# Kernel optimization log

Measured on AMD Instinct MI355X. Metric: run time of the kernel, lower is better.

The kernel has to match this reference:

```python
import jax, jax.numpy as jnp
import numpy as np

B, T, C, H = 2, 2048, 1024, 16
HD = C // H  # head_size = 64
EPS = 1e-5


def setup_inputs() -> dict:
    key = jax.random.key(0)
    ks = jax.random.split(key, 12)
    s = lambda fan_in: 1.0 / np.sqrt(fan_in)
    return {
        "x": jax.random.normal(ks[0], (B, T, C), jnp.float32),
        # attention projections, stored [in, out] so y = x @ W
        "Wq": jax.random.normal(ks[1], (C, C), jnp.float32) * s(C),
        "Wk": jax.random.normal(ks[2], (C, C), jnp.float32) * s(C),
        "Wv": jax.random.normal(ks[3], (C, C), jnp.float32) * s(C),
        "Wo": jax.random.normal(ks[4], (C, C), jnp.float32) * s(C),
        "bo": jnp.zeros((C,), jnp.float32),
        "ln1_g": jnp.ones((C,), jnp.float32),
        "ln1_b": jnp.zeros((C,), jnp.float32),
        "ln2_g": jnp.ones((C,), jnp.float32),
        "ln2_b": jnp.zeros((C,), jnp.float32),
        "W1": jax.random.normal(ks[5], (C, 4 * C), jnp.float32) * s(C),
        "b1": jnp.zeros((4 * C,), jnp.float32),
        "W2": jax.random.normal(ks[6], (4 * C, C), jnp.float32) * s(4 * C),
        "b2": jnp.zeros((C,), jnp.float32),
    }


def _layernorm(x, g, b):
    mu = jnp.mean(x, axis=-1, keepdims=True)
    var = jnp.mean(jnp.square(x - mu), axis=-1, keepdims=True)
    return (x - mu) * jax.lax.rsqrt(var + EPS) * g + b


def reference(x, Wq, Wk, Wv, Wo, bo, ln1_g, ln1_b, ln2_g, ln2_b, W1, b1, W2, b2):
    # Dropout layers are inference no-ops (eval mode).
    Bz, Tz, Cz = x.shape
    h = _layernorm(x, ln1_g, ln1_b)
    # fused multi-head projections (equivalent to per-head Linears concatenated)
    q = (h @ Wq).reshape(Bz, Tz, H, HD)
    k = (h @ Wk).reshape(Bz, Tz, H, HD)
    v = (h @ Wv).reshape(Bz, Tz, H, HD)
    scores = jnp.einsum("bqhd,bkhd->bhqk", q, k) / np.sqrt(HD).astype(np.float32)
    causal = jnp.tril(jnp.ones((Tz, Tz), bool))
    scores = jnp.where(causal, scores, -jnp.inf)
    attn = jax.nn.softmax(scores, axis=-1)
    out = jnp.einsum("bhqk,bkhd->bqhd", attn, v).reshape(Bz, Tz, Cz)
    x = x + out @ Wo + bo
    h2 = _layernorm(x, ln2_g, ln2_b)
    ff = jax.nn.relu(h2 @ W1 + b1) @ W2 + b2
    return x + ff
```

## Files before the change

kernel.cpp:

```cpp
#include <hip/hip_runtime.h>
#include <hip/hip_bf16.h>
#include <stdint.h>

#define B_  2
#define T_  2048
#define C_  1024
#define H_  16
#define HD_ 64
#define M_  4096
#define FF_ 4096

typedef unsigned short ushort_t;
typedef __bf16 bf16x8 __attribute__((ext_vector_type(8)));
typedef float  f32x4  __attribute__((ext_vector_type(4)));
typedef float  f32x16 __attribute__((ext_vector_type(16)));
typedef unsigned int u32x2 __attribute__((ext_vector_type(2)));
typedef unsigned int u32x4 __attribute__((ext_vector_type(4)));

#define C2_ 0.1803368801111204f

__device__ inline ushort_t f2bf(float f) {
  uint32_t u = __builtin_bit_cast(uint32_t, f);
  u += 0x7fffu + ((u >> 16) & 1u);
  return (ushort_t)(u >> 16);
}
__device__ inline uint32_t pk2(float lo, float hi) {
  return (uint32_t)f2bf(lo) | ((uint32_t)f2bf(hi) << 16);
}

__device__ inline void gload_lds16(const void* g, void* l) {
  __builtin_amdgcn_global_load_lds(
      (const __attribute__((address_space(1))) uint32_t*)g,
      (__attribute__((address_space(3))) uint32_t*)l, 16, 0, 0);
}

__device__ inline int qswz(int row, int byte_in_row) {
  return row * 128 + (byte_in_row ^ ((row & 7) << 4));
}

__global__ __launch_bounds__(256) void lnorm_kernel(
    const float* __restrict__ x, const float* __restrict__ g,
    const float* __restrict__ b, ushort_t* __restrict__ o) {
  int row = blockIdx.x;
  int tid = threadIdx.x;
  const float4* xr = (const float4*)(x + (size_t)row * C_);
  float4 xv = xr[tid];
  float s  = xv.x + xv.y + xv.z + xv.w;
  float s2 = xv.x*xv.x + xv.y*xv.y + xv.z*xv.z + xv.w*xv.w;
#pragma unroll
  for (int off = 32; off; off >>= 1) {
    s  += __shfl_down(s,  off);
    s2 += __shfl_down(s2, off);
  }
  __shared__ float rs[4], rq[4];
  int wid = tid >> 6;
  if ((tid & 63) == 0) { rs[wid] = s; rq[wid] = s2; }
  __syncthreads();
  float tot  = rs[0] + rs[1] + rs[2] + rs[3];
  float tot2 = rq[0] + rq[1] + rq[2] + rq[3];
  float mu   = tot * (1.0f / C_);
  float var  = tot2 * (1.0f / C_) - mu * mu;
  float rstd = rsqrtf(var + 1e-5f);
  float4 gv = ((const float4*)g)[tid];
  float4 bv = ((const float4*)b)[tid];
  float y0 = (xv.x - mu) * rstd * gv.x + bv.x;
  float y1 = (xv.y - mu) * rstd * gv.y + bv.y;
  float y2 = (xv.z - mu) * rstd * gv.z + bv.z;
  float y3 = (xv.w - mu) * rstd * gv.w + bv.w;
  uint2 pk;
  pk.x = (uint32_t)f2bf(y0) | ((uint32_t)f2bf(y1) << 16);
  pk.y = (uint32_t)f2bf(y2) | ((uint32_t)f2bf(y3) << 16);
  *(uint2*)(o + (size_t)row * C_ + tid * 4) = pk;
}

__global__ __launch_bounds__(256) void tcast_kernel(
    const float* __restrict__ W, ushort_t* __restrict__ Wt, int K, int N) {
  __shared__ float t[32][33];
  int bn = blockIdx.x, bk = blockIdx.y;
  int tx = threadIdx.x & 31, ty = threadIdx.x >> 5;
#pragma unroll
  for (int i = 0; i < 4; ++i)
    t[ty + i*8][tx] = W[(size_t)(bk*32 + ty + i*8) * N + bn*32 + tx];
  __syncthreads();
#pragma unroll
  for (int i = 0; i < 4; ++i)
    Wt[(size_t)(bn*32 + ty + i*8) * K + bk*32 + tx] = f2bf(t[tx][ty + i*8]);
}

__global__ __launch_bounds__(256) void vtrans_kernel(
    const ushort_t* __restrict__ qkv, ushort_t* __restrict__ vt) {
  __shared__ ushort_t t[32][33];
  int tt = blockIdx.x;
  int cc = blockIdx.y;
  int bb = blockIdx.z;
  int tx = threadIdx.x & 31, ty = threadIdx.x >> 5;
#pragma unroll
  for (int i = 0; i < 4; ++i)
    t[ty + i*8][tx] = qkv[(size_t)(bb*T_ + tt*32 + ty + i*8)*3072 + 2048 + cc*32 + tx];
  __syncthreads();
  int crow = threadIdx.x >> 4;
  int ucol = threadIdx.x & 15;
#pragma unroll
  for (int i = 0; i < 2; ++i) {
    int c = crow + i*16;
    uint32_t vlo = t[ucol*2][c], vhi = t[ucol*2 + 1][c];
    *(uint32_t*)&vt[(size_t)(bb*1024 + cc*32 + c)*T_ + tt*32 + ucol*2] =
        vlo | (vhi << 16);
  }
}

template<int BIAS, int RELU, int RESID, int OUTBF16>
__global__ __launch_bounds__(256) void gemm_kernel(
    const ushort_t* __restrict__ A, const ushort_t* __restrict__ Bt,
    const float* __restrict__ bias, const float* __restrict__ resid,
    void* __restrict__ outp, int M, int N, int K) {
  __shared__ __align__(16) ushort_t As[128*32];
  __shared__ __align__(16) ushort_t Bs[128*32];
  int bn = blockIdx.x, bm = blockIdx.y;
  int tid = threadIdx.x;
  int lane = tid & 63, wid = tid >> 6;
  int wr = (wid >> 1) * 64, wc = (wid & 1) * 64;
  int r = lane & 15, g = lane >> 4;
  int srow = tid >> 2, scc = (tid & 3) * 8;
  int srow2 = srow + 64;
  f32x4 acc[4][4] = {};
  int nk = K >> 5;
  for (int kt = 0; kt < nk; ++kt) {
    gload_lds16(&A[(size_t)(bm*128 + srow)  * K + kt*32 + scc], &As[tid*8]);
    gload_lds16(&A[(size_t)(bm*128 + srow2) * K + kt*32 + scc], &As[(tid+256)*8]);
    gload_lds16(&Bt[(size_t)(bn*128 + srow)  * K + kt*32 + scc], &Bs[tid*8]);
    gload_lds16(&Bt[(size_t)(bn*128 + srow2) * K + kt*32 + scc], &Bs[(tid+256)*8]);
    __syncthreads();
    bf16x8 af[4], bfv[4];
#pragma unroll
    for (int m = 0; m < 4; ++m)
      af[m] = *(const bf16x8*)&As[(wr + m*16 + r)*32 + g*8];
#pragma unroll
    for (int n = 0; n < 4; ++n)
      bfv[n] = *(const bf16x8*)&Bs[(wc + n*16 + r)*32 + g*8];
#pragma unroll
    for (int m = 0; m < 4; ++m)
#pragma unroll
      for (int n = 0; n < 4; ++n)
        acc[m][n] = __builtin_amdgcn_mfma_f32_16x16x32_bf16(
            af[m], bfv[n], acc[m][n], 0, 0, 0);
    __syncthreads();
  }
#pragma unroll
  for (int m = 0; m < 4; ++m)
#pragma unroll
    for (int n = 0; n < 4; ++n)
#pragma unroll
      for (int e = 0; e < 4; ++e) {
        int row = bm*128 + wr + m*16 + g*4 + e;
        int col = bn*128 + wc + n*16 + r;
        float v = acc[m][n][e];
        if (BIAS)  v += bias[col];
        if (RESID) v += resid[(size_t)row * N + col];
        if (RELU)  v = fmaxf(v, 0.0f);
        if (OUTBF16) ((ushort_t*)outp)[(size_t)row * N + col] = f2bf(v);
        else         ((float*)outp)[(size_t)row * N + col]    = v;
      }
}

__global__ __launch_bounds__(256) void attn_kernel(
    const ushort_t* __restrict__ q, const ushort_t* __restrict__ k,
    const ushort_t* __restrict__ vt, ushort_t* __restrict__ o, int ldq) {
  int bid = blockIdx.x;
  int qbb = 15 - (bid & 15);
  int hh = (bid >> 4) & 15;
  int bb = bid >> 8;
  __shared__ __align__(16) ushort_t Ks[64*64];
  __shared__ __align__(16) ushort_t Vts[64*64];
  int tid = threadIdx.x, lane = tid & 63, w = tid >> 6;
  int qi = lane & 31, hi = lane >> 5;
  int qrow0 = qbb*128 + w*32;
  int qg = qrow0 + qi;
  int lt = 2*qbb + (w >> 1);
  int nkv = 2*qbb + 2;

  const ushort_t* qbase = q + ((size_t)(bb*T_ + qg))*ldq + hh*64;
  bf16x8 qv[4];
#pragma unroll
  for (int c = 0; c < 4; ++c)
    qv[c] = *(const bf16x8*)(qbase + c*16 + hi*8);

  const ushort_t* kbase = k  + ((size_t)bb*T_)*ldq + hh*64;
  const ushort_t* vbase = vt + ((size_t)(bb*1024 + hh*64))*T_;

  int r0s = tid >> 3;
  int s0  = ((tid & 7) ^ (r0s & 7)) * 8;

  f32x16 O0 = {}, O1 = {};
  float mrun = -1e30f, lrun = 0.f;

  for (int kt = 0; kt < nkv; ++kt) {
    gload_lds16(kbase + ((size_t)(kt*64 + r0s))*ldq + s0,      &Ks[tid*8]);
    gload_lds16(kbase + ((size_t)(kt*64 + r0s + 32))*ldq + s0, &Ks[(tid+256)*8]);
    gload_lds16(vbase + (size_t)r0s*T_ + kt*64 + s0,           &Vts[tid*8]);
    gload_lds16(vbase + (size_t)(r0s+32)*T_ + kt*64 + s0,      &Vts[(tid+256)*8]);
    __syncthreads();
    if (kt <= lt) {
      f32x16 a0 = {}, a1 = {};
#pragma unroll
      for (int c = 0; c < 4; ++c) {
        bf16x8 k0 = *(const bf16x8*)((char*)Ks + qswz(qi,      c*32 + hi*16));
        bf16x8 k1 = *(const bf16x8*)((char*)Ks + qswz(32 + qi, c*32 + hi*16));
        a0 = __builtin_amdgcn_mfma_f32_32x32x16_bf16(k0, qv[c], a0, 0, 0, 0);
        a1 = __builtin_amdgcn_mfma_f32_32x32x16_bf16(k1, qv[c], a1, 0, 0, 0);
      }
      if (kt == lt) {
        int kof = kt*64 + 4*hi;
#pragma unroll
        for (int rg = 0; rg < 16; ++rg) {
          int kp = kof + (rg & 3) + 8*(rg >> 2);
          if (kp > qg)      a0[rg] = -1e30f;
          if (kp + 32 > qg) a1[rg] = -1e30f;
        }
      }
      float tm = -1e30f;
#pragma unroll
      for (int rg = 0; rg < 16; ++rg) tm = fmaxf(tm, fmaxf(a0[rg], a1[rg]));
      tm = fmaxf(tm, __shfl_xor(tm, 32));
      float mnew = fmaxf(mrun, tm);
      float sf = exp2f((mrun - mnew) * C2_);
      mrun = mnew;
      float mc = mnew * C2_;
#pragma unroll
      for (int rg = 0; rg < 16; ++rg) {
        a0[rg] = exp2f(a0[rg]*C2_ - mc);
        a1[rg] = exp2f(a1[rg]*C2_ - mc);
      }
      float rs = 0.f;
#pragma unroll
      for (int rg = 0; rg < 16; ++rg) rs += a0[rg] + a1[rg];
      rs += __shfl_xor(rs, 32);
      lrun = lrun*sf + rs;
#pragma unroll
      for (int rg = 0; rg < 16; ++rg) { O0[rg] *= sf; O1[rg] *= sf; }
      bf16x8 pf[4];
#pragma unroll
      for (int kb = 0; kb < 2; ++kb)
#pragma unroll
        for (int jj = 0; jj < 2; ++jj) {
          int rb = jj*8;
          float v0 = kb ? a1[rb+0] : a0[rb+0], v1 = kb ? a1[rb+1] : a0[rb+1];
          float v2 = kb ? a1[rb+2] : a0[rb+2], v3 = kb ? a1[rb+3] : a0[rb+3];
          float v4 = kb ? a1[rb+4] : a0[rb+4], v5 = kb ? a1[rb+5] : a0[rb+5];
          float v6 = kb ? a1[rb+6] : a0[rb+6], v7 = kb ? a1[rb+7] : a0[rb+7];
          uint32_t d0 = pk2(v0, v1), d1 = pk2(v2, v3);
          uint32_t e0 = pk2(v4, v5), e1 = pk2(v6, v7);
          uint32_t pd0 = __shfl_xor(d0, 32), pd1 = __shfl_xor(d1, 32);
          uint32_t pe0 = __shfl_xor(e0, 32), pe1 = __shfl_xor(e1, 32);
          u32x4 fw;
          fw[0] = hi ? pe0 : d0;
          fw[1] = hi ? pe1 : d1;
          fw[2] = hi ? e0  : pd0;
          fw[3] = hi ? e1  : pd1;
          pf[kb*2 + jj] = __builtin_bit_cast(bf16x8, fw);
        }
#pragma unroll
      for (int kk = 0; kk < 4; ++kk) {
        bf16x8 vv0 = *(const bf16x8*)((char*)Vts + qswz(qi,      kk*32 + hi*16));
        bf16x8 vv1 = *(const bf16x8*)((char*)Vts + qswz(32 + qi, kk*32 + hi*16));
        O0 = __builtin_amdgcn_mfma_f32_32x32x16_bf16(vv0, pf[kk], O0, 0, 0, 0);
        O1 = __builtin_amdgcn_mfma_f32_32x32x16_bf16(vv1, pf[kk], O1, 0, 0, 0);
      }
    }
    __syncthreads();
  }
  float inv = 1.0f / lrun;
  ushort_t* ob = o + ((size_t)(bb*T_ + qg))*C_ + hh*64;
#pragma unroll
  for (int tq = 0; tq < 4; ++tq) {
    u32x2 st0, st1;
    st0[0] = pk2(O0[4*tq+0]*inv, O0[4*tq+1]*inv);
    st0[1] = pk2(O0[4*tq+2]*inv, O0[4*tq+3]*inv);
    st1[0] = pk2(O1[4*tq+0]*inv, O1[4*tq+1]*inv);
    st1[1] = pk2(O1[4*tq+2]*inv, O1[4*tq+3]*inv);
    *(u32x2*)(ob + 8*tq + 4*hi)      = st0;
    *(u32x2*)(ob + 32 + 8*tq + 4*hi) = st1;
  }
}

extern "C" void kernel_launch(void* const* d_in, const int* in_sizes, int n_in,
                              void* d_out, int out_size, void* d_ws, size_t ws_size,
                              hipStream_t stream) {
  const float* x    = (const float*)d_in[0];
  const float* Wq   = (const float*)d_in[1];
  const float* Wk   = (const float*)d_in[2];
  const float* Wv   = (const float*)d_in[3];
  const float* Wo   = (const float*)d_in[4];
  const float* bo   = (const float*)d_in[5];
  const float* ln1g = (const float*)d_in[6];
  const float* ln1b = (const float*)d_in[7];
  const float* ln2g = (const float*)d_in[8];
  const float* ln2b = (const float*)d_in[9];
  const float* W1   = (const float*)d_in[10];
  const float* b1   = (const float*)d_in[11];
  const float* W2   = (const float*)d_in[12];
  const float* b2   = (const float*)d_in[13];

  char* ws = (char*)d_ws;
  ushort_t* h    = (ushort_t*)(ws + ((size_t)0  << 20));
  ushort_t* vt   = (ushort_t*)(ws + ((size_t)0  << 20));
  ushort_t* qkv  = (ushort_t*)(ws + ((size_t)8  << 20));
  ushort_t* ff   = (ushort_t*)(ws + ((size_t)0  << 20));
  ushort_t* attn = (ushort_t*)(ws + ((size_t)32 << 20));
  float*    x2   = (float*)   (ws + ((size_t)40 << 20));
  ushort_t* h2   = (ushort_t*)(ws + ((size_t)56 << 20));
  ushort_t* wqt  = (ushort_t*)(ws + ((size_t)64 << 20));
  ushort_t* wkt  = (ushort_t*)(ws + ((size_t)66 << 20));
  ushort_t* wvt  = (ushort_t*)(ws + ((size_t)68 << 20));
  ushort_t* wot  = (ushort_t*)(ws + ((size_t)70 << 20));
  ushort_t* w1t  = (ushort_t*)(ws + ((size_t)72 << 20));
  ushort_t* w2t  = (ushort_t*)(ws + ((size_t)80 << 20));
  float* out = (float*)d_out;

  tcast_kernel<<<dim3(32, 32),  256, 0, stream>>>(Wq, wqt, 1024, 1024);
  tcast_kernel<<<dim3(32, 32),  256, 0, stream>>>(Wk, wkt, 1024, 1024);
  tcast_kernel<<<dim3(32, 32),  256, 0, stream>>>(Wv, wvt, 1024, 1024);
  tcast_kernel<<<dim3(32, 32),  256, 0, stream>>>(Wo, wot, 1024, 1024);
  tcast_kernel<<<dim3(128, 32), 256, 0, stream>>>(W1, w1t, 1024, 4096);
  tcast_kernel<<<dim3(32, 128), 256, 0, stream>>>(W2, w2t, 4096, 1024);

  lnorm_kernel<<<M_, 256, 0, stream>>>(x, ln1g, ln1b, h);

  gemm_kernel<0,0,0,1><<<dim3(24, 32), 256, 0, stream>>>(h, wqt, nullptr, nullptr, qkv, M_, 3*C_, C_);

  vtrans_kernel<<<dim3(64, 32, 2), 256, 0, stream>>>(qkv, vt);

  attn_kernel<<<512, 256, 0, stream>>>(qkv, qkv + C_, vt, attn, 3*C_);

  gemm_kernel<1,0,1,0><<<dim3(8, 32), 256, 0, stream>>>(attn, wot, bo, x, x2, M_, C_, C_);

  lnorm_kernel<<<M_, 256, 0, stream>>>(x2, ln2g, ln2b, h2);

  gemm_kernel<1,1,0,1><<<dim3(32, 32), 256, 0, stream>>>(h2, w1t, b1, nullptr, ff, M_, FF_, C_);

  gemm_kernel<1,0,1,0><<<dim3(8, 32), 256, 0, stream>>>(ff, w2t, b2, x2, out, M_, C_, FF_);
}
```

Before: 457.0 us.

## Double-buffer GEMM LDS tiles and use narrower N tiles for C-output GEMMs

The GEMM kernel now keeps two LDS buffers and issues the global-to-LDS loads for the next K tile before computing on the current one, so load latency can overlap with MFMA work and one barrier per iteration is dropped. A BN template parameter lets the two GEMMs with 1024 output columns use 64-wide N tiles, which doubles their grid from 256 to 512 blocks to fill more CUs. The cost is double the LDS per block, which may lower occupancy, and less reuse of the A tile in the narrow-tile case.

```diff
diff --git a/kernel.cpp b/kernel.cpp
--- a/kernel.cpp
+++ b/kernel.cpp
@@ -109,51 +109,68 @@
   }
 }
 
-template<int BIAS, int RELU, int RESID, int OUTBF16>
+template<int BN, int BIAS, int RELU, int RESID, int OUTBF16>
 __global__ __launch_bounds__(256) void gemm_kernel(
     const ushort_t* __restrict__ A, const ushort_t* __restrict__ Bt,
     const float* __restrict__ bias, const float* __restrict__ resid,
     void* __restrict__ outp, int M, int N, int K) {
-  __shared__ __align__(16) ushort_t As[128*32];
-  __shared__ __align__(16) ushort_t Bs[128*32];
+  constexpr int NFR = BN / 32;
+  __shared__ __align__(16) ushort_t As[2][128*32];
+  __shared__ __align__(16) ushort_t Bs[2][BN*32];
   int bn = blockIdx.x, bm = blockIdx.y;
   int tid = threadIdx.x;
   int lane = tid & 63, wid = tid >> 6;
-  int wr = (wid >> 1) * 64, wc = (wid & 1) * 64;
+  int wr = (wid >> 1) * 64, wc = (wid & 1) * (BN / 2);
   int r = lane & 15, g = lane >> 4;
   int srow = tid >> 2, scc = (tid & 3) * 8;
-  int srow2 = srow + 64;
-  f32x4 acc[4][4] = {};
+  f32x4 acc[4][NFR] = {};
   int nk = K >> 5;
+
+  const ushort_t* Abase = A  + (size_t)(bm*128) * K;
+  const ushort_t* Bbase = Bt + (size_t)(bn*BN) * K;
+
+#define STAGE_(bi, kt_)                                                        \
+  do {                                                                         \
+    gload_lds16(Abase + (size_t)srow * K + (kt_)*32 + scc, &As[bi][tid*8]);    \
+    gload_lds16(Abase + (size_t)(srow + 64) * K + (kt_)*32 + scc,              \
+                &As[bi][(tid + 256)*8]);                                       \
+    gload_lds16(Bbase + (size_t)srow * K + (kt_)*32 + scc, &Bs[bi][tid*8]);    \
+    if (BN == 128)                                                             \
+      gload_lds16(Bbase + (size_t)(srow + 64) * K + (kt_)*32 + scc,            \
+                  &Bs[bi][(tid + 256)*8]);                                     \
+  } while (0)
+
+  STAGE_(0, 0);
+  __syncthreads();
+  int buf = 0;
   for (int kt = 0; kt < nk; ++kt) {
-    gload_lds16(&A[(size_t)(bm*128 + srow)  * K + kt*32 + scc], &As[tid*8]);
-    gload_lds16(&A[(size_t)(bm*128 + srow2) * K + kt*32 + scc], &As[(tid+256)*8]);
-    gload_lds16(&Bt[(size_t)(bn*128 + srow)  * K + kt*32 + scc], &Bs[tid*8]);
-    gload_lds16(&Bt[(size_t)(bn*128 + srow2) * K + kt*32 + scc], &Bs[(tid+256)*8]);
-    __syncthreads();
-    bf16x8 af[4], bfv[4];
+    if (kt + 1 < nk) STAGE_(buf ^ 1, kt + 1);
+    bf16x8 af[4], bfv[NFR];
 #pragma unroll
     for (int m = 0; m < 4; ++m)
-      af[m] = *(const bf16x8*)&As[(wr + m*16 + r)*32 + g*8];
-#pragma unroll
-    for (int n = 0; n < 4; ++n)
-      bfv[n] = *(const bf16x8*)&Bs[(wc + n*16 + r)*32 + g*8];
+      af[m] = *(const bf16x8*)&As[buf][(wr + m*16 + r)*32 + g*8];
+#pragma unroll
+    for (int n = 0; n < NFR; ++n)
+      bfv[n] = *(const bf16x8*)&Bs[buf][(wc + n*16 + r)*32 + g*8];
 #pragma unroll
     for (int m = 0; m < 4; ++m)
 #pragma unroll
-      for (int n = 0; n < 4; ++n)
+      for (int n = 0; n < NFR; ++n)
         acc[m][n] = __builtin_amdgcn_mfma_f32_16x16x32_bf16(
             af[m], bfv[n], acc[m][n], 0, 0, 0);
     __syncthreads();
-  }
+    buf ^= 1;
+  }
+#undef STAGE_
+
 #pragma unroll
   for (int m = 0; m < 4; ++m)
 #pragma unroll
-    for (int n = 0; n < 4; ++n)
+    for (int n = 0; n < NFR; ++n)
 #pragma unroll
       for (int e = 0; e < 4; ++e) {
         int row = bm*128 + wr + m*16 + g*4 + e;
-        int col = bn*128 + wc + n*16 + r;
+        int col = bn*BN + wc + n*16 + r;
         float v = acc[m][n][e];
         if (BIAS)  v += bias[col];
         if (RESID) v += resid[(size_t)row * N + col];
@@ -326,17 +343,17 @@
 
   lnorm_kernel<<<M_, 256, 0, stream>>>(x, ln1g, ln1b, h);
 
-  gemm_kernel<0,0,0,1><<<dim3(24, 32), 256, 0, stream>>>(h, wqt, nullptr, nullptr, qkv, M_, 3*C_, C_);
+  gemm_kernel<128,0,0,0,1><<<dim3(24, 32), 256, 0, stream>>>(h, wqt, nullptr, nullptr, qkv, M_, 3*C_, C_);
 
   vtrans_kernel<<<dim3(64, 32, 2), 256, 0, stream>>>(qkv, vt);
 
   attn_kernel<<<512, 256, 0, stream>>>(qkv, qkv + C_, vt, attn, 3*C_);
 
-  gemm_kernel<1,0,1,0><<<dim3(8, 32), 256, 0, stream>>>(attn, wot, bo, x, x2, M_, C_, C_);
+  gemm_kernel<64,1,0,1,0><<<dim3(16, 32), 256, 0, stream>>>(attn, wot, bo, x, x2, M_, C_, C_);
 
   lnorm_kernel<<<M_, 256, 0, stream>>>(x2, ln2g, ln2b, h2);
 
-  gemm_kernel<1,1,0,1><<<dim3(32, 32), 256, 0, stream>>>(h2, w1t, b1, nullptr, ff, M_, FF_, C_);
-
-  gemm_kernel<1,0,1,0><<<dim3(8, 32), 256, 0, stream>>>(ff, w2t, b2, x2, out, M_, C_, FF_);
-}
+  gemm_kernel<128,1,1,0,1><<<dim3(32, 32), 256, 0, stream>>>(h2, w1t, b1, nullptr, ff, M_, FF_, C_);
+
+  gemm_kernel<64,1,0,1,0><<<dim3(16, 32), 256, 0, stream>>>(ff, w2t, b2, x2, out, M_, C_, FF_);
+}
```

New measurement: 421.8 us. 7.7% less time.
